# Performance work log

Measured on AMD Instinct MI355X. Metric: run time of the kernel, lower is better.

Reference implementation:

```python
import jax, jax.numpy as jnp
import numpy as np

N = 320
C_Z = 128
H = 4
C_H = 32


def setup_inputs() -> dict:
    key = jax.random.key(0)
    ks = jax.random.split(key, 9)
    s = 0.02
    return {
        "x_normed": jax.random.normal(ks[0], (1, N, N, C_Z), dtype=jnp.float32),
        "triangle_bias": jax.random.normal(ks[1], (1, 1, H, N, N), dtype=jnp.float32),
        "wq": jax.random.normal(ks[2], (C_Z, H * C_H), dtype=jnp.float32) * s,
        "wk": jax.random.normal(ks[3], (C_Z, H * C_H), dtype=jnp.float32) * s,
        "wv": jax.random.normal(ks[4], (C_Z, H * C_H), dtype=jnp.float32) * s,
        "wg": jax.random.normal(ks[5], (C_Z, H * C_H), dtype=jnp.float32) * s,
        "bg": jnp.ones((H * C_H,), dtype=jnp.float32),  # OpenFold gating bias init = 1
        "wo": jax.random.normal(ks[6], (H * C_H, C_Z), dtype=jnp.float32) * s,
        "bo": jnp.zeros((C_Z,), dtype=jnp.float32),
    }


def reference(x_normed, triangle_bias, wq, wk, wv, wg, bg, wo, bo):
    b, n, m, cz = x_normed.shape  # [1, N, N, C_Z]
    # q/k/v projections (no bias, per OpenFold Attention)
    q = (x_normed @ wq).reshape(b, n, m, H, C_H) / np.sqrt(C_H)
    k = (x_normed @ wk).reshape(b, n, m, H, C_H)
    v = (x_normed @ wv).reshape(b, n, m, H, C_H)
    # attention over the last row dim; first N is a batch dim.
    # scores: [b, n, H, q, k]; triangle_bias [1, 1, H, N, N] broadcasts over n.
    scores = jnp.einsum("bnqhc,bnkhc->bnhqk", q, k) + triangle_bias
    a = jax.nn.softmax(scores, axis=-1)
    o = jnp.einsum("bnhqk,bnkhc->bnqhc", a, v)
    # sigmoid output gating
    g = jax.nn.sigmoid((x_normed @ wg + bg).reshape(b, n, m, H, C_H))
    o = o * g
    out = o.reshape(b, n, m, H * C_H) @ wo + bo
    return out
```

## Files before the change

kernel.cpp:

```cpp
#include <hip/hip_runtime.h>

typedef __bf16 bf16;
typedef __bf16 bf16x8 __attribute__((ext_vector_type(8)));
typedef __bf16 bf16x4 __attribute__((ext_vector_type(4)));
typedef __bf16 bf16x2 __attribute__((ext_vector_type(2)));
typedef float  f32x4  __attribute__((ext_vector_type(4)));
typedef unsigned int u32;
typedef u32 u32x4 __attribute__((ext_vector_type(4)));

#define NN_  320
#define CZ_  128
#define H_   4
#define CH_  32

__device__ __forceinline__ u32 pack_bf16(float a, float b) {
    bf16x2 t; t[0] = (bf16)a; t[1] = (bf16)b;
    return __builtin_bit_cast(u32, t);
}

__global__ __launch_bounds__(512) void qkvg_kernel(
    const float* __restrict__ x,
    const float* __restrict__ wq, const float* __restrict__ wk,
    const float* __restrict__ wv, const float* __restrict__ wg,
    const float* __restrict__ bg,
    bf16* __restrict__ Qp, bf16* __restrict__ Kp,
    bf16* __restrict__ Vp, bf16* __restrict__ Gp)
{
    __shared__ bf16 wl[128][136];
    const int tid  = threadIdx.x;
    const int lane = tid & 63, wid = tid >> 6;
    const int l15  = lane & 15, l4 = lane >> 4;
    const int m0   = blockIdx.x << 7;

    const int arow = m0 + wid * 16 + l15;
    bf16x8 xf[4];
    #pragma unroll
    for (int ks = 0; ks < 4; ++ks) {
        float4 f0 = *reinterpret_cast<const float4*>(x + (size_t)arow * CZ_ + ks * 32 + l4 * 8);
        float4 f1 = *reinterpret_cast<const float4*>(x + (size_t)arow * CZ_ + ks * 32 + l4 * 8 + 4);
        bf16x8 t;
        t[0]=(bf16)f0.x; t[1]=(bf16)f0.y; t[2]=(bf16)f0.z; t[3]=(bf16)f0.w;
        t[4]=(bf16)f1.x; t[5]=(bf16)f1.y; t[6]=(bf16)f1.z; t[7]=(bf16)f1.w;
        xf[ks] = t;
    }

    int nQ[4], qQ[4];
    #pragma unroll
    for (int r = 0; r < 4; ++r) {
        int m = m0 + wid * 16 + l4 * 4 + r;
        nQ[r] = m / NN_; qQ[r] = m - nQ[r] * NN_;
    }
    const int nV = arow / NN_, qV = arow - nV * NN_;

    const float* Ws[4] = {wq, wk, wv, wg};
    #pragma unroll
    for (int mat = 0; mat < 4; ++mat) {
        __syncthreads();
        const float* w = Ws[mat];
        #pragma unroll
        for (int it = 0; it < 8; ++it) {
            int u  = tid + (it << 9);
            int j  = u & 127, k4 = u >> 7;
            bf16x4 t;
            t[0] = (bf16)w[(k4 * 4 + 0) * CZ_ + j];
            t[1] = (bf16)w[(k4 * 4 + 1) * CZ_ + j];
            t[2] = (bf16)w[(k4 * 4 + 2) * CZ_ + j];
            t[3] = (bf16)w[(k4 * 4 + 3) * CZ_ + j];
            *reinterpret_cast<bf16x4*>(&wl[j][k4 * 4]) = t;
        }
        __syncthreads();

        f32x4 zero = {0.f, 0.f, 0.f, 0.f};
        f32x4 acc[8];
        #pragma unroll
        for (int ct = 0; ct < 8; ++ct) acc[ct] = zero;

        #pragma unroll
        for (int ks = 0; ks < 4; ++ks) {
            #pragma unroll
            for (int ct = 0; ct < 8; ++ct) {
                bf16x8 wf = *reinterpret_cast<const bf16x8*>(&wl[ct * 16 + l15][ks * 32 + l4 * 8]);
                if (mat == 2)
                    acc[ct] = __builtin_amdgcn_mfma_f32_16x16x32_bf16(wf, xf[ks], acc[ct], 0, 0, 0);
                else
                    acc[ct] = __builtin_amdgcn_mfma_f32_16x16x32_bf16(xf[ks], wf, acc[ct], 0, 0, 0);
            }
        }

        if (mat == 0) {
            #pragma unroll
            for (int ct = 0; ct < 8; ++ct) {
                const int cout = ct * 16 + l15, hh = cout >> 5, cc = cout & 31;
                #pragma unroll
                for (int r = 0; r < 4; ++r)
                    Qp[(size_t)((nQ[r] * H_ + hh) * NN_ + qQ[r]) * CH_ + cc] =
                        (bf16)(acc[ct][r] * 0.17677669529663687f);
            }
        } else if (mat == 1) {
            #pragma unroll
            for (int ct = 0; ct < 8; ++ct) {
                const int cout = ct * 16 + l15, hh = cout >> 5, cc = cout & 31;
                #pragma unroll
                for (int r = 0; r < 4; ++r)
                    Kp[(size_t)((nQ[r] * H_ + hh) * NN_ + qQ[r]) * CH_ + cc] = (bf16)acc[ct][r];
            }
        } else if (mat == 2) {
            #pragma unroll
            for (int ct = 0; ct < 8; ++ct) {
                #pragma unroll
                for (int r = 0; r < 4; ++r) {
                    const int cout = ct * 16 + l4 * 4 + r, hh = cout >> 5, cc = cout & 31;
                    Vp[(size_t)((nV * H_ + hh) * CH_ + cc) * NN_ + qV] = (bf16)acc[ct][r];
                }
            }
        } else {
            #pragma unroll
            for (int ct = 0; ct < 8; ++ct) {
                const int cout = ct * 16 + l15;
                const float bgj = bg[cout];
                #pragma unroll
                for (int r = 0; r < 4; ++r) {
                    float t = acc[ct][r] + bgj;
                    Gp[(size_t)(m0 + wid * 16 + l4 * 4 + r) * CZ_ + cout] =
                        (bf16)(1.0f / (1.0f + __expf(-t)));
                }
            }
        }
    }
}

__global__ __launch_bounds__(640, 2) void attn_kernel(
    const bf16* __restrict__ Qp, const bf16* __restrict__ Kp,
    const bf16* __restrict__ Vp, bf16* __restrict__ Gp,
    const float* __restrict__ bias)
{
    __shared__ bf16 Kl[320][40];
    __shared__ bf16 Vl[32][344];
    const int tid  = threadIdx.x;
    const int lane = tid & 63;
    const int wid  = tid >> 6;
    const int l15  = lane & 15, l4 = lane >> 4;
    const int gid = blockIdx.x;
    const int lin = (gid & 7) * 160 + (gid >> 3);
    const int h   = lin / NN_;
    const int n   = lin - h * NN_;

    const size_t nh = (size_t)(n * H_ + h);
    const bf16* Kh = Kp + nh * NN_ * CH_;
    const bf16* Vh = Vp + nh * CH_ * NN_;
    const bf16* Qh = Qp + nh * NN_ * CH_;

    #pragma unroll
    for (int i = 0; i < 2; ++i) {
        int c  = tid + i * 640;
        int kr = c >> 2, kc = (c & 3) * 8;
        *reinterpret_cast<bf16x8*>(&Kl[kr][kc]) =
            *reinterpret_cast<const bf16x8*>(Kh + kr * CH_ + kc);
        int vr = c / 40, vc = (c % 40) * 8;
        *reinterpret_cast<bf16x8*>(&Vl[vr][vc]) =
            *reinterpret_cast<const bf16x8*>(Vh + vr * NN_ + vc);
    }
    __syncthreads();

    const f32x4 zero = {0.f, 0.f, 0.f, 0.f};

    #pragma unroll
    for (int qg = 0; qg < 2; ++qg) {
        const int qb = wid * 32 + qg * 16;
        const bf16x8 qf = *reinterpret_cast<const bf16x8*>(&Qh[(qb + l15) * CH_ + l4 * 8]);
        const float* bq = bias + ((size_t)h * NN_ + qb + l15) * NN_ + l4 * 4;
        const size_t gbase = ((size_t)n * NN_ + qb + l15) * CZ_ + h * CH_;
        const bf16x4 g0 = *reinterpret_cast<const bf16x4*>(&Gp[gbase + l4 * 4]);
        const bf16x4 g1 = *reinterpret_cast<const bf16x4*>(&Gp[gbase + 16 + l4 * 4]);

        f32x4 o0 = zero, o1 = zero;
        float lsum = 0.f;
        float4 bp0 = *reinterpret_cast<const float4*>(bq);
        float4 bp1 = *reinterpret_cast<const float4*>(bq + 16);

        #pragma unroll 2
        for (int tp = 0; tp < 10; ++tp) {
            const int kvm = tp * 32;
            bf16x8 kf0 = *reinterpret_cast<const bf16x8*>(&Kl[kvm + l15][l4 * 8]);
            bf16x8 kf1 = *reinterpret_cast<const bf16x8*>(&Kl[kvm + 16 + l15][l4 * 8]);
            f32x4 s0 = __builtin_amdgcn_mfma_f32_16x16x32_bf16(kf0, qf, zero, 0, 0, 0);
            f32x4 s1 = __builtin_amdgcn_mfma_f32_16x16x32_bf16(kf1, qf, zero, 0, 0, 0);
            float4 b0 = bp0, b1 = bp1;
            if (tp < 9) {
                bp0 = *reinterpret_cast<const float4*>(bq + (tp + 1) * 32);
                bp1 = *reinterpret_cast<const float4*>(bq + (tp + 1) * 32 + 16);
            }
            float p0 = __expf(s0[0] + b0.x);
            float p1 = __expf(s0[1] + b0.y);
            float p2 = __expf(s0[2] + b0.z);
            float p3 = __expf(s0[3] + b0.w);
            float p4 = __expf(s1[0] + b1.x);
            float p5 = __expf(s1[1] + b1.y);
            float p6 = __expf(s1[2] + b1.z);
            float p7 = __expf(s1[3] + b1.w);
            lsum += ((p0 + p1) + (p2 + p3)) + ((p4 + p5) + (p6 + p7));
            u32x4 ww;
            ww[0] = pack_bf16(p0, p1);
            ww[1] = pack_bf16(p2, p3);
            ww[2] = pack_bf16(p4, p5);
            ww[3] = pack_bf16(p6, p7);
            bf16x8 pf = __builtin_bit_cast(bf16x8, ww);

            bf16x4 va0 = *reinterpret_cast<const bf16x4*>(&Vl[l15][kvm + l4 * 4]);
            bf16x4 va1 = *reinterpret_cast<const bf16x4*>(&Vl[l15][kvm + 16 + l4 * 4]);
            bf16x4 vb0 = *reinterpret_cast<const bf16x4*>(&Vl[16 + l15][kvm + l4 * 4]);
            bf16x4 vb1 = *reinterpret_cast<const bf16x4*>(&Vl[16 + l15][kvm + 16 + l4 * 4]);
            bf16x8 vf0 = __builtin_shufflevector(va0, va1, 0, 1, 2, 3, 4, 5, 6, 7);
            bf16x8 vf1 = __builtin_shufflevector(vb0, vb1, 0, 1, 2, 3, 4, 5, 6, 7);

            o0 = __builtin_amdgcn_mfma_f32_16x16x32_bf16(vf0, pf, o0, 0, 0, 0);
            o1 = __builtin_amdgcn_mfma_f32_16x16x32_bf16(vf1, pf, o1, 0, 0, 0);
        }

        float l = lsum;
        l += __shfl_xor(l, 16);
        l += __shfl_xor(l, 32);
        const float linv = 1.0f / l;

        bf16x4 h0, h1;
        #pragma unroll
        for (int r = 0; r < 4; ++r) {
            h0[r] = (bf16)(o0[r] * linv * (float)g0[r]);
            h1[r] = (bf16)(o1[r] * linv * (float)g1[r]);
        }
        *reinterpret_cast<bf16x4*>(&Gp[gbase + l4 * 4]) = h0;
        *reinterpret_cast<bf16x4*>(&Gp[gbase + 16 + l4 * 4]) = h1;
    }
}

__global__ __launch_bounds__(512) void oproj_kernel(
    const bf16* __restrict__ og, const float* __restrict__ wo,
    const float* __restrict__ bo, float* __restrict__ out)
{
    __shared__ bf16 wl[128][136];
    const int tid  = threadIdx.x;
    const int lane = tid & 63, wid = tid >> 6;
    const int l15  = lane & 15, l4 = lane >> 4;
    const int m0   = blockIdx.x << 7;

    #pragma unroll
    for (int it = 0; it < 8; ++it) {
        int u  = tid + (it << 9);
        int j  = u & 127, k4 = u >> 7;
        bf16x4 t;
        t[0] = (bf16)wo[(k4 * 4 + 0) * CZ_ + j];
        t[1] = (bf16)wo[(k4 * 4 + 1) * CZ_ + j];
        t[2] = (bf16)wo[(k4 * 4 + 2) * CZ_ + j];
        t[3] = (bf16)wo[(k4 * 4 + 3) * CZ_ + j];
        *reinterpret_cast<bf16x4*>(&wl[j][k4 * 4]) = t;
    }
    __syncthreads();

    const int arow = m0 + wid * 16 + l15;
    bf16x8 af[4];
    #pragma unroll
    for (int ks = 0; ks < 4; ++ks)
        af[ks] = *reinterpret_cast<const bf16x8*>(&og[(size_t)arow * CZ_ + ks * 32 + l4 * 8]);

    f32x4 zero = {0.f, 0.f, 0.f, 0.f};
    f32x4 acc[8];
    #pragma unroll
    for (int ct = 0; ct < 8; ++ct) acc[ct] = zero;
    #pragma unroll
    for (int ks = 0; ks < 4; ++ks)
        #pragma unroll
        for (int ct = 0; ct < 8; ++ct) {
            bf16x8 wf = *reinterpret_cast<const bf16x8*>(&wl[ct * 16 + l15][ks * 32 + l4 * 8]);
            acc[ct] = __builtin_amdgcn_mfma_f32_16x16x32_bf16(af[ks], wf, acc[ct], 0, 0, 0);
        }

    #pragma unroll
    for (int ct = 0; ct < 8; ++ct) {
        const int cout = ct * 16 + l15;
        const float bov = bo[cout];
        #pragma unroll
        for (int r = 0; r < 4; ++r)
            out[(size_t)(m0 + wid * 16 + l4 * 4 + r) * CZ_ + cout] = acc[ct][r] + bov;
    }
}

extern "C" void kernel_launch(void* const* d_in, const int* in_sizes, int n_in,
                              void* d_out, int out_size, void* d_ws, size_t ws_size,
                              hipStream_t stream) {
    (void)in_sizes; (void)n_in; (void)out_size; (void)ws_size;
    const float* x    = (const float*)d_in[0];
    const float* bias = (const float*)d_in[1];
    const float* wq   = (const float*)d_in[2];
    const float* wk   = (const float*)d_in[3];
    const float* wv   = (const float*)d_in[4];
    const float* wg   = (const float*)d_in[5];
    const float* bg   = (const float*)d_in[6];
    const float* wo   = (const float*)d_in[7];
    const float* bo   = (const float*)d_in[8];
    float* out = (float*)d_out;

    const size_t ELEMS = (size_t)NN_ * NN_ * CZ_;
    bf16* Qp = (bf16*)d_ws;
    bf16* Gp = Qp + ELEMS;
    bf16* Kp = (bf16*)d_out;
    bf16* Vp = Kp + ELEMS;

    qkvg_kernel<<<dim3(800), 512, 0, stream>>>(x, wq, wk, wv, wg, bg, Qp, Kp, Vp, Gp);
    attn_kernel<<<dim3(1280), 640, 0, stream>>>(Qp, Kp, Vp, Gp, bias);
    oproj_kernel<<<dim3(800), 512, 0, stream>>>(Gp, wo, bo, out);
}
```

Baseline: 147.3 us.

## Split attention blocks into query halves and interleave two query tiles per wave

Each attention block now handles half of the 320 query rows of one (n, head) pair, using 320 threads instead of 640, and the grid doubles to 2560. Each wave processes its two 16-row query tiles together in one loop, sharing the K and V fragment reads from LDS across both tiles. The bias prefetch becomes a two-deep double buffer. The costs are that K and V are now loaded into LDS twice per (n, head) pair and that per-thread register pressure rises; the V LDS padding also changes.

Result: slower. 151.1 us (+2.6%).

```diff
diff --git a/kernel.cpp b/kernel.cpp
--- a/kernel.cpp
+++ b/kernel.cpp
@@ -129,21 +129,23 @@
     }
 }
 
-__global__ __launch_bounds__(640, 2) void attn_kernel(
+__global__ __launch_bounds__(320, 4) void attn_kernel(
     const bf16* __restrict__ Qp, const bf16* __restrict__ Kp,
     const bf16* __restrict__ Vp, bf16* __restrict__ Gp,
     const float* __restrict__ bias)
 {
     __shared__ bf16 Kl[320][40];
-    __shared__ bf16 Vl[32][344];
+    __shared__ bf16 Vl[32][328];
     const int tid  = threadIdx.x;
     const int lane = tid & 63;
     const int wid  = tid >> 6;
     const int l15  = lane & 15, l4 = lane >> 4;
     const int gid = blockIdx.x;
-    const int lin = (gid & 7) * 160 + (gid >> 3);
-    const int h   = lin / NN_;
-    const int n   = lin - h * NN_;
+    const int lin = (gid & 7) * 320 + (gid >> 3);
+    const int h   = lin / 640;
+    const int rem = lin - h * 640;
+    const int n   = rem >> 1;
+    const int qh  = (rem & 1) * 160;
 
     const size_t nh = (size_t)(n * H_ + h);
     const bf16* Kh = Kp + nh * NN_ * CH_;
@@ -151,8 +153,8 @@
     const bf16* Qh = Qp + nh * NN_ * CH_;
 
     #pragma unroll
-    for (int i = 0; i < 2; ++i) {
-        int c  = tid + i * 640;
+    for (int i = 0; i < 4; ++i) {
+        int c  = tid + i * 320;
         int kr = c >> 2, kc = (c & 3) * 8;
         *reinterpret_cast<bf16x8*>(&Kl[kr][kc]) =
             *reinterpret_cast<const bf16x8*>(Kh + kr * CH_ + kc);
@@ -162,75 +164,115 @@
     }
     __syncthreads();
 
+    const int qb0 = qh + wid * 32;
+    const int qb1 = qb0 + 16;
+    const bf16x8 qf0 = *reinterpret_cast<const bf16x8*>(&Qh[(qb0 + l15) * CH_ + l4 * 8]);
+    const bf16x8 qf1 = *reinterpret_cast<const bf16x8*>(&Qh[(qb1 + l15) * CH_ + l4 * 8]);
+    const float* bp0 = bias + ((size_t)h * NN_ + qb0 + l15) * NN_ + l4 * 4;
+    const float* bp1 = bias + ((size_t)h * NN_ + qb1 + l15) * NN_ + l4 * 4;
+    const size_t gb0 = ((size_t)n * NN_ + qb0 + l15) * CZ_ + h * CH_;
+    const size_t gb1 = ((size_t)n * NN_ + qb1 + l15) * CZ_ + h * CH_;
+    const bf16x4 g00 = *reinterpret_cast<const bf16x4*>(&Gp[gb0 + l4 * 4]);
+    const bf16x4 g01 = *reinterpret_cast<const bf16x4*>(&Gp[gb0 + 16 + l4 * 4]);
+    const bf16x4 g10 = *reinterpret_cast<const bf16x4*>(&Gp[gb1 + l4 * 4]);
+    const bf16x4 g11 = *reinterpret_cast<const bf16x4*>(&Gp[gb1 + 16 + l4 * 4]);
+
     const f32x4 zero = {0.f, 0.f, 0.f, 0.f};
-
-    #pragma unroll
-    for (int qg = 0; qg < 2; ++qg) {
-        const int qb = wid * 32 + qg * 16;
-        const bf16x8 qf = *reinterpret_cast<const bf16x8*>(&Qh[(qb + l15) * CH_ + l4 * 8]);
-        const float* bq = bias + ((size_t)h * NN_ + qb + l15) * NN_ + l4 * 4;
-        const size_t gbase = ((size_t)n * NN_ + qb + l15) * CZ_ + h * CH_;
-        const bf16x4 g0 = *reinterpret_cast<const bf16x4*>(&Gp[gbase + l4 * 4]);
-        const bf16x4 g1 = *reinterpret_cast<const bf16x4*>(&Gp[gbase + 16 + l4 * 4]);
-
-        f32x4 o0 = zero, o1 = zero;
-        float lsum = 0.f;
-        float4 bp0 = *reinterpret_cast<const float4*>(bq);
-        float4 bp1 = *reinterpret_cast<const float4*>(bq + 16);
-
-        #pragma unroll 2
-        for (int tp = 0; tp < 10; ++tp) {
-            const int kvm = tp * 32;
-            bf16x8 kf0 = *reinterpret_cast<const bf16x8*>(&Kl[kvm + l15][l4 * 8]);
-            bf16x8 kf1 = *reinterpret_cast<const bf16x8*>(&Kl[kvm + 16 + l15][l4 * 8]);
-            f32x4 s0 = __builtin_amdgcn_mfma_f32_16x16x32_bf16(kf0, qf, zero, 0, 0, 0);
-            f32x4 s1 = __builtin_amdgcn_mfma_f32_16x16x32_bf16(kf1, qf, zero, 0, 0, 0);
-            float4 b0 = bp0, b1 = bp1;
-            if (tp < 9) {
-                bp0 = *reinterpret_cast<const float4*>(bq + (tp + 1) * 32);
-                bp1 = *reinterpret_cast<const float4*>(bq + (tp + 1) * 32 + 16);
-            }
-            float p0 = __expf(s0[0] + b0.x);
-            float p1 = __expf(s0[1] + b0.y);
-            float p2 = __expf(s0[2] + b0.z);
-            float p3 = __expf(s0[3] + b0.w);
-            float p4 = __expf(s1[0] + b1.x);
-            float p5 = __expf(s1[1] + b1.y);
-            float p6 = __expf(s1[2] + b1.z);
-            float p7 = __expf(s1[3] + b1.w);
-            lsum += ((p0 + p1) + (p2 + p3)) + ((p4 + p5) + (p6 + p7));
-            u32x4 ww;
-            ww[0] = pack_bf16(p0, p1);
-            ww[1] = pack_bf16(p2, p3);
-            ww[2] = pack_bf16(p4, p5);
-            ww[3] = pack_bf16(p6, p7);
-            bf16x8 pf = __builtin_bit_cast(bf16x8, ww);
-
-            bf16x4 va0 = *reinterpret_cast<const bf16x4*>(&Vl[l15][kvm + l4 * 4]);
-            bf16x4 va1 = *reinterpret_cast<const bf16x4*>(&Vl[l15][kvm + 16 + l4 * 4]);
-            bf16x4 vb0 = *reinterpret_cast<const bf16x4*>(&Vl[16 + l15][kvm + l4 * 4]);
-            bf16x4 vb1 = *reinterpret_cast<const bf16x4*>(&Vl[16 + l15][kvm + 16 + l4 * 4]);
-            bf16x8 vf0 = __builtin_shufflevector(va0, va1, 0, 1, 2, 3, 4, 5, 6, 7);
-            bf16x8 vf1 = __builtin_shufflevector(vb0, vb1, 0, 1, 2, 3, 4, 5, 6, 7);
-
-            o0 = __builtin_amdgcn_mfma_f32_16x16x32_bf16(vf0, pf, o0, 0, 0, 0);
-            o1 = __builtin_amdgcn_mfma_f32_16x16x32_bf16(vf1, pf, o1, 0, 0, 0);
-        }
-
-        float l = lsum;
-        l += __shfl_xor(l, 16);
-        l += __shfl_xor(l, 32);
-        const float linv = 1.0f / l;
-
-        bf16x4 h0, h1;
-        #pragma unroll
-        for (int r = 0; r < 4; ++r) {
-            h0[r] = (bf16)(o0[r] * linv * (float)g0[r]);
-            h1[r] = (bf16)(o1[r] * linv * (float)g1[r]);
-        }
-        *reinterpret_cast<bf16x4*>(&Gp[gbase + l4 * 4]) = h0;
-        *reinterpret_cast<bf16x4*>(&Gp[gbase + 16 + l4 * 4]) = h1;
-    }
+    f32x4 o00 = zero, o01 = zero, o10 = zero, o11 = zero;
+    float ls0 = 0.f, ls1 = 0.f;
+
+    float4 bA[4], bB[4];
+    bA[0] = *reinterpret_cast<const float4*>(bp0);
+    bA[1] = *reinterpret_cast<const float4*>(bp0 + 16);
+    bA[2] = *reinterpret_cast<const float4*>(bp1);
+    bA[3] = *reinterpret_cast<const float4*>(bp1 + 16);
+    bB[0] = *reinterpret_cast<const float4*>(bp0 + 32);
+    bB[1] = *reinterpret_cast<const float4*>(bp0 + 48);
+    bB[2] = *reinterpret_cast<const float4*>(bp1 + 32);
+    bB[3] = *reinterpret_cast<const float4*>(bp1 + 48);
+
+#define ATTN_TP(TP, BUF, PRE)                                                      \
+    {                                                                              \
+        const int kvm = (TP) * 32;                                                 \
+        bf16x8 kf0 = *reinterpret_cast<const bf16x8*>(&Kl[kvm + l15][l4 * 8]);     \
+        bf16x8 kf1 = *reinterpret_cast<const bf16x8*>(&Kl[kvm + 16 + l15][l4 * 8]);\
+        f32x4 s00 = __builtin_amdgcn_mfma_f32_16x16x32_bf16(kf0, qf0, zero, 0, 0, 0); \
+        f32x4 s01 = __builtin_amdgcn_mfma_f32_16x16x32_bf16(kf1, qf0, zero, 0, 0, 0); \
+        f32x4 s10 = __builtin_amdgcn_mfma_f32_16x16x32_bf16(kf0, qf1, zero, 0, 0, 0); \
+        f32x4 s11 = __builtin_amdgcn_mfma_f32_16x16x32_bf16(kf1, qf1, zero, 0, 0, 0); \
+        float e0 = __expf(s00[0] + BUF[0].x);                                      \
+        float e1 = __expf(s00[1] + BUF[0].y);                                      \
+        float e2 = __expf(s00[2] + BUF[0].z);                                      \
+        float e3 = __expf(s00[3] + BUF[0].w);                                      \
+        float e4 = __expf(s01[0] + BUF[1].x);                                      \
+        float e5 = __expf(s01[1] + BUF[1].y);                                      \
+        float e6 = __expf(s01[2] + BUF[1].z);                                      \
+        float e7 = __expf(s01[3] + BUF[1].w);                                      \
+        ls0 += ((e0 + e1) + (e2 + e3)) + ((e4 + e5) + (e6 + e7));                  \
+        u32x4 w0;                                                                  \
+        w0[0] = pack_bf16(e0, e1); w0[1] = pack_bf16(e2, e3);                      \
+        w0[2] = pack_bf16(e4, e5); w0[3] = pack_bf16(e6, e7);                      \
+        bf16x8 pf0 = __builtin_bit_cast(bf16x8, w0);                               \
+        float f0 = __expf(s10[0] + BUF[2].x);                                      \
+        float f1 = __expf(s10[1] + BUF[2].y);                                      \
+        float f2 = __expf(s10[2] + BUF[2].z);                                      \
+        float f3 = __expf(s10[3] + BUF[2].w);                                      \
+        float f4 = __expf(s11[0] + BUF[3].x);                                      \
+        float f5 = __expf(s11[1] + BUF[3].y);                                      \
+        float f6 = __expf(s11[2] + BUF[3].z);                                      \
+        float f7 = __expf(s11[3] + BUF[3].w);                                      \
+        ls1 += ((f0 + f1) + (f2 + f3)) + ((f4 + f5) + (f6 + f7));                  \
+        u32x4 w1;                                                                  \
+        w1[0] = pack_bf16(f0, f1); w1[1] = pack_bf16(f2, f3);                      \
+        w1[2] = pack_bf16(f4, f5); w1[3] = pack_bf16(f6, f7);                      \
+        bf16x8 pf1 = __builtin_bit_cast(bf16x8, w1);                               \
+        if (PRE) {                 \
+            BUF[0] = *reinterpret_cast<const float4*>(bp0 + ((TP) + 2) * 32);      \
+            BUF[1] = *reinterpret_cast<const float4*>(bp0 + ((TP) + 2) * 32 + 16); \
+            BUF[2] = *reinterpret_cast<const float4*>(bp1 + ((TP) + 2) * 32);      \
+            BUF[3] = *reinterpret_cast<const float4*>(bp1 + ((TP) + 2) * 32 + 16); \
+        }                                                                          \
+        bf16x4 va0 = *reinterpret_cast<const bf16x4*>(&Vl[l15][kvm + l4 * 4]);     \
+        bf16x4 va1 = *reinterpret_cast<const bf16x4*>(&Vl[l15][kvm + 16 + l4 * 4]);\
+        bf16x4 vb0 = *reinterpret_cast<const bf16x4*>(&Vl[16 + l15][kvm + l4 * 4]);\
+        bf16x4 vb1 = *reinterpret_cast<const bf16x4*>(&Vl[16 + l15][kvm + 16 + l4 * 4]); \
+        bf16x8 vf0 = __builtin_shufflevector(va0, va1, 0, 1, 2, 3, 4, 5, 6, 7);    \
+        bf16x8 vf1 = __builtin_shufflevector(vb0, vb1, 0, 1, 2, 3, 4, 5, 6, 7);    \
+        o00 = __builtin_amdgcn_mfma_f32_16x16x32_bf16(vf0, pf0, o00, 0, 0, 0);     \
+        o01 = __builtin_amdgcn_mfma_f32_16x16x32_bf16(vf1, pf0, o01, 0, 0, 0);     \
+        o10 = __builtin_amdgcn_mfma_f32_16x16x32_bf16(vf0, pf1, o10, 0, 0, 0);     \
+        o11 = __builtin_amdgcn_mfma_f32_16x16x32_bf16(vf1, pf1, o11, 0, 0, 0);     \
+    }
+
+    #pragma unroll 1
+    for (int t2 = 0; t2 < 4; ++t2) {
+        const int tp0 = 2 * t2;
+        ATTN_TP(tp0, bA, true);
+        ATTN_TP(tp0 + 1, bB, true);
+    }
+    ATTN_TP(8, bA, false);
+    ATTN_TP(9, bB, false);
+#undef ATTN_TP
+
+    ls0 += __shfl_xor(ls0, 16);
+    ls0 += __shfl_xor(ls0, 32);
+    ls1 += __shfl_xor(ls1, 16);
+    ls1 += __shfl_xor(ls1, 32);
+    const float li0 = 1.0f / ls0;
+    const float li1 = 1.0f / ls1;
+
+    bf16x4 h00, h01, h10, h11;
+    #pragma unroll
+    for (int r = 0; r < 4; ++r) {
+        h00[r] = (bf16)(o00[r] * li0 * (float)g00[r]);
+        h01[r] = (bf16)(o01[r] * li0 * (float)g01[r]);
+        h10[r] = (bf16)(o10[r] * li1 * (float)g10[r]);
+        h11[r] = (bf16)(o11[r] * li1 * (float)g11[r]);
+    }
+    *reinterpret_cast<bf16x4*>(&Gp[gb0 + l4 * 4]) = h00;
+    *reinterpret_cast<bf16x4*>(&Gp[gb0 + 16 + l4 * 4]) = h01;
+    *reinterpret_cast<bf16x4*>(&Gp[gb1 + l4 * 4]) = h10;
+    *reinterpret_cast<bf16x4*>(&Gp[gb1 + 16 + l4 * 4]) = h11;
 }
 
 __global__ __launch_bounds__(512) void oproj_kernel(
@@ -306,6 +348,6 @@
     bf16* Vp = Kp + ELEMS;
 
     qkvg_kernel<<<dim3(800), 512, 0, stream>>>(x, wq, wk, wv, wg, bg, Qp, Kp, Vp, Gp);
-    attn_kernel<<<dim3(1280), 640, 0, stream>>>(Qp, Kp, Vp, Gp, bias);
+    attn_kernel<<<dim3(2560), 320, 0, stream>>>(Qp, Kp, Vp, Gp, bias);
     oproj_kernel<<<dim3(800), 512, 0, stream>>>(Gp, wo, bo, out);
 }
```

## Use exp2 with folded log2e, MFMA row-sum, and two-deep bias prefetch

Applied to the files above, without the earlier changes.

Folds log2(e) into the Q scale and bias FMA so the softmax uses the native exp2 instruction. The row sum is now computed by an extra MFMA against a ones vector, which replaces the scalar adds and cross-lane shuffles. The bias prefetch is two tiles deep, with explicit unrolling and s_setprio around the MFMAs. Together these aim to cut VALU work and hide the latency of the global bias loads, at the cost of one extra MFMA per tile and a row sum taken from bf16-rounded probabilities.

Result: faster. 143.0 us (-3.0%).

```diff
diff --git a/kernel.cpp b/kernel.cpp
--- a/kernel.cpp
+++ b/kernel.cpp
@@ -12,6 +12,7 @@
 #define CZ_  128
 #define H_   4
 #define CH_  32
+#define LOG2E_ 1.4426950408889634f
 
 __device__ __forceinline__ u32 pack_bf16(float a, float b) {
     bf16x2 t; t[0] = (bf16)a; t[1] = (bf16)b;
@@ -94,7 +95,7 @@
                 #pragma unroll
                 for (int r = 0; r < 4; ++r)
                     Qp[(size_t)((nQ[r] * H_ + hh) * NN_ + qQ[r]) * CH_ + cc] =
-                        (bf16)(acc[ct][r] * 0.17677669529663687f);
+                        (bf16)(acc[ct][r] * 0.25500003540695464f);
             }
         } else if (mat == 1) {
             #pragma unroll
@@ -163,8 +164,11 @@
     __syncthreads();
 
     const f32x4 zero = {0.f, 0.f, 0.f, 0.f};
-
-    #pragma unroll
+    bf16x8 onesf;
+    #pragma unroll
+    for (int i = 0; i < 8; ++i) onesf[i] = (bf16)1.0f;
+
+    #pragma unroll 1
     for (int qg = 0; qg < 2; ++qg) {
         const int qb = wid * 32 + qg * 16;
         const bf16x8 qf = *reinterpret_cast<const bf16x8*>(&Qh[(qb + l15) * CH_ + l4 * 8]);
@@ -173,54 +177,61 @@
         const bf16x4 g0 = *reinterpret_cast<const bf16x4*>(&Gp[gbase + l4 * 4]);
         const bf16x4 g1 = *reinterpret_cast<const bf16x4*>(&Gp[gbase + 16 + l4 * 4]);
 
-        f32x4 o0 = zero, o1 = zero;
-        float lsum = 0.f;
-        float4 bp0 = *reinterpret_cast<const float4*>(bq);
-        float4 bp1 = *reinterpret_cast<const float4*>(bq + 16);
-
-        #pragma unroll 2
-        for (int tp = 0; tp < 10; ++tp) {
-            const int kvm = tp * 32;
-            bf16x8 kf0 = *reinterpret_cast<const bf16x8*>(&Kl[kvm + l15][l4 * 8]);
-            bf16x8 kf1 = *reinterpret_cast<const bf16x8*>(&Kl[kvm + 16 + l15][l4 * 8]);
-            f32x4 s0 = __builtin_amdgcn_mfma_f32_16x16x32_bf16(kf0, qf, zero, 0, 0, 0);
-            f32x4 s1 = __builtin_amdgcn_mfma_f32_16x16x32_bf16(kf1, qf, zero, 0, 0, 0);
-            float4 b0 = bp0, b1 = bp1;
-            if (tp < 9) {
-                bp0 = *reinterpret_cast<const float4*>(bq + (tp + 1) * 32);
-                bp1 = *reinterpret_cast<const float4*>(bq + (tp + 1) * 32 + 16);
-            }
-            float p0 = __expf(s0[0] + b0.x);
-            float p1 = __expf(s0[1] + b0.y);
-            float p2 = __expf(s0[2] + b0.z);
-            float p3 = __expf(s0[3] + b0.w);
-            float p4 = __expf(s1[0] + b1.x);
-            float p5 = __expf(s1[1] + b1.y);
-            float p6 = __expf(s1[2] + b1.z);
-            float p7 = __expf(s1[3] + b1.w);
-            lsum += ((p0 + p1) + (p2 + p3)) + ((p4 + p5) + (p6 + p7));
-            u32x4 ww;
-            ww[0] = pack_bf16(p0, p1);
-            ww[1] = pack_bf16(p2, p3);
-            ww[2] = pack_bf16(p4, p5);
-            ww[3] = pack_bf16(p6, p7);
-            bf16x8 pf = __builtin_bit_cast(bf16x8, ww);
-
-            bf16x4 va0 = *reinterpret_cast<const bf16x4*>(&Vl[l15][kvm + l4 * 4]);
-            bf16x4 va1 = *reinterpret_cast<const bf16x4*>(&Vl[l15][kvm + 16 + l4 * 4]);
-            bf16x4 vb0 = *reinterpret_cast<const bf16x4*>(&Vl[16 + l15][kvm + l4 * 4]);
-            bf16x4 vb1 = *reinterpret_cast<const bf16x4*>(&Vl[16 + l15][kvm + 16 + l4 * 4]);
-            bf16x8 vf0 = __builtin_shufflevector(va0, va1, 0, 1, 2, 3, 4, 5, 6, 7);
-            bf16x8 vf1 = __builtin_shufflevector(vb0, vb1, 0, 1, 2, 3, 4, 5, 6, 7);
-
-            o0 = __builtin_amdgcn_mfma_f32_16x16x32_bf16(vf0, pf, o0, 0, 0, 0);
-            o1 = __builtin_amdgcn_mfma_f32_16x16x32_bf16(vf1, pf, o1, 0, 0, 0);
-        }
-
-        float l = lsum;
-        l += __shfl_xor(l, 16);
-        l += __shfl_xor(l, 32);
-        const float linv = 1.0f / l;
+        f32x4 o0 = zero, o1 = zero, ol = zero;
+
+        float4 bA0 = *reinterpret_cast<const float4*>(bq);
+        float4 bA1 = *reinterpret_cast<const float4*>(bq + 16);
+        float4 bB0 = *reinterpret_cast<const float4*>(bq + 32);
+        float4 bB1 = *reinterpret_cast<const float4*>(bq + 48);
+
+#define ATTN_TP(TP, B0, B1, PRE)                                                   \
+    {                                                                              \
+        const int kvm = (TP) * 32;                                                 \
+        bf16x8 kf0 = *reinterpret_cast<const bf16x8*>(&Kl[kvm + l15][l4 * 8]);     \
+        bf16x8 kf1 = *reinterpret_cast<const bf16x8*>(&Kl[kvm + 16 + l15][l4 * 8]);\
+        __builtin_amdgcn_s_setprio(1);                                             \
+        f32x4 s0 = __builtin_amdgcn_mfma_f32_16x16x32_bf16(kf0, qf, zero, 0, 0, 0);\
+        f32x4 s1 = __builtin_amdgcn_mfma_f32_16x16x32_bf16(kf1, qf, zero, 0, 0, 0);\
+        __builtin_amdgcn_s_setprio(0);                                             \
+        float p0 = __builtin_amdgcn_exp2f(__builtin_fmaf(B0.x, LOG2E_, s0[0]));    \
+        float p1 = __builtin_amdgcn_exp2f(__builtin_fmaf(B0.y, LOG2E_, s0[1]));    \
+        float p2 = __builtin_amdgcn_exp2f(__builtin_fmaf(B0.z, LOG2E_, s0[2]));    \
+        float p3 = __builtin_amdgcn_exp2f(__builtin_fmaf(B0.w, LOG2E_, s0[3]));    \
+        float p4 = __builtin_amdgcn_exp2f(__builtin_fmaf(B1.x, LOG2E_, s1[0]));    \
+        float p5 = __builtin_amdgcn_exp2f(__builtin_fmaf(B1.y, LOG2E_, s1[1]));    \
+        float p6 = __builtin_amdgcn_exp2f(__builtin_fmaf(B1.z, LOG2E_, s1[2]));    \
+        float p7 = __builtin_amdgcn_exp2f(__builtin_fmaf(B1.w, LOG2E_, s1[3]));    \
+        u32x4 ww;                                                                  \
+        ww[0] = pack_bf16(p0, p1); ww[1] = pack_bf16(p2, p3);                      \
+        ww[2] = pack_bf16(p4, p5); ww[3] = pack_bf16(p6, p7);                      \
+        bf16x8 pf = __builtin_bit_cast(bf16x8, ww);                                \
+        if (PRE) {                                            \
+            B0 = *reinterpret_cast<const float4*>(bq + ((TP) + 2) * 32);           \
+            B1 = *reinterpret_cast<const float4*>(bq + ((TP) + 2) * 32 + 16);      \
+        }                                                                          \
+        bf16x4 va0 = *reinterpret_cast<const bf16x4*>(&Vl[l15][kvm + l4 * 4]);     \
+        bf16x4 va1 = *reinterpret_cast<const bf16x4*>(&Vl[l15][kvm + 16 + l4 * 4]);\
+        bf16x4 vb0 = *reinterpret_cast<const bf16x4*>(&Vl[16 + l15][kvm + l4 * 4]);\
+        bf16x4 vb1 = *reinterpret_cast<const bf16x4*>(&Vl[16 + l15][kvm + 16 + l4 * 4]); \
+        bf16x8 vf0 = __builtin_shufflevector(va0, va1, 0, 1, 2, 3, 4, 5, 6, 7);    \
+        bf16x8 vf1 = __builtin_shufflevector(vb0, vb1, 0, 1, 2, 3, 4, 5, 6, 7);    \
+        __builtin_amdgcn_s_setprio(1);                                             \
+        ol = __builtin_amdgcn_mfma_f32_16x16x32_bf16(onesf, pf, ol, 0, 0, 0);      \
+        o0 = __builtin_amdgcn_mfma_f32_16x16x32_bf16(vf0, pf, o0, 0, 0, 0);        \
+        o1 = __builtin_amdgcn_mfma_f32_16x16x32_bf16(vf1, pf, o1, 0, 0, 0);        \
+        __builtin_amdgcn_s_setprio(0);                                             \
+    }
+
+        #pragma unroll 1
+        for (int t2 = 0; t2 < 4; ++t2) {
+            ATTN_TP(2 * t2,     bA0, bA1, true);
+            ATTN_TP(2 * t2 + 1, bB0, bB1, true);
+        }
+        ATTN_TP(8, bA0, bA1, false);
+        ATTN_TP(9, bB0, bB1, false);
+#undef ATTN_TP
+
+        const float linv = 1.0f / ol[0];
 
         bf16x4 h0, h1;
         #pragma unroll
```
